# Performance work log

Hardware: AMD Instinct MI355X
Metric: run time of the kernel (lower is better)

Reference implementation:

```python
import jax, jax.numpy as jnp
import numpy as np

N, B, E, H, L, NF = 32768, 2048, 524288, 128, 7, 10
NODE_F = 60  # 10 frames * (loc 3 + vel 3)
OUT_F = 30   # 10 frames * 3


def _mlp(x, W1, b1, W2, b2):
    return jax.nn.relu(x @ W1 + b1) @ W2 + b2


def _lin(key, fan_in, fan_out):
    s = 1.0 / np.sqrt(fan_in)
    kw, kb = jax.random.split(key)
    W = jax.random.uniform(kw, (fan_in, fan_out), jnp.float32, -s, s)
    b = jax.random.uniform(kb, (fan_out,), jnp.float32, -s, s)
    return W, b


def setup_inputs() -> dict:
    key = jax.random.key(0)
    ks = jax.random.split(key, 12)
    p = {}
    p["loc"] = jax.random.normal(ks[0], (N, NF, 3), jnp.float32)
    p["vel"] = jax.random.normal(ks[1], (N, NF, 3), jnp.float32)
    p["y"] = jax.random.normal(ks[2], (N, NF, 3), jnp.float32)
    p["edge_index"] = jax.random.randint(ks[3], (2, E), 0, N, dtype=jnp.int64)
    p["batch_size"] = B
    # embedder: Linear(60,H) -> ReLU -> Linear(H,H)
    p["emb_W1"], p["emb_b1"] = _lin(ks[4], NODE_F, H)
    p["emb_W2"], p["emb_b2"] = _lin(ks[5], H, H)
    # per-layer message net Linear(2H,H)->ReLU->Linear(H,H); update net Linear(2H,H)->ReLU->Linear(H,H)
    mW1, mb1, mW2, mb2, uW1, ub1, uW2, ub2 = [], [], [], [], [], [], [], []
    for i in range(L):
        k = jax.random.fold_in(ks[6], i)
        k1, k2, k3, k4 = jax.random.split(k, 4)
        a, b = _lin(k1, 2 * H, H); mW1.append(a); mb1.append(b)
        a, b = _lin(k2, H, H); mW2.append(a); mb2.append(b)
        a, b = _lin(k3, 2 * H, H); uW1.append(a); ub1.append(b)
        a, b = _lin(k4, H, H); uW2.append(a); ub2.append(b)
    p["msg_W1"] = jnp.stack(mW1); p["msg_b1"] = jnp.stack(mb1)
    p["msg_W2"] = jnp.stack(mW2); p["msg_b2"] = jnp.stack(mb2)
    p["upd_W1"] = jnp.stack(uW1); p["upd_b1"] = jnp.stack(ub1)
    p["upd_W2"] = jnp.stack(uW2); p["upd_b2"] = jnp.stack(ub2)
    # head: Linear(H,H) -> ReLU -> Linear(H,30)
    p["head_W1"], p["head_b1"] = _lin(ks[7], H, H)
    p["head_W2"], p["head_b2"] = _lin(ks[8], H, OUT_F)
    return p


def reference(loc, vel, y, edge_index, batch_size,
              emb_W1, emb_b1, emb_W2, emb_b2,
              msg_W1, msg_b1, msg_W2, msg_b2,
              upd_W1, upd_b1, upd_W2, upd_b2,
              head_W1, head_b1, head_W2, head_b2):
    n = loc.shape[0]
    src, dst = edge_index[0], edge_index[1]  # x_j = x[src], x_i = x[dst] (PyG source_to_target)
    x = jnp.concatenate([loc, vel], axis=-1).reshape(n, -1)  # (N, 60)
    x = _mlp(x, emb_W1, emb_b1, emb_W2, emb_b2)              # (N, H)
    for i in range(L):
        m_in = jnp.concatenate([x[dst], x[src]], axis=-1)    # (E, 2H) cat(x_i, x_j)
        msg = _mlp(m_in, msg_W1[i], msg_b1[i], msg_W2[i], msg_b2[i])  # (E, H)
        agg = jax.ops.segment_sum(msg, dst, num_segments=n)  # scatter-add at targets
        x = _mlp(jnp.concatenate([x, agg], axis=-1), upd_W1[i], upd_b1[i], upd_W2[i], upd_b2[i])
    x = _mlp(x, head_W1, head_b1, head_W2, head_b2)          # (N, 30)
    loc_pred = x.reshape(n, NF, 3) + loc
    d = jnp.sqrt(jnp.sum((loc_pred - y) ** 2, axis=-1))      # (N, NF)
    ade_loss = d.reshape(batch_size, -1, NF).mean(axis=-1).mean(axis=-1)  # (B,)
    fde = jnp.sqrt(jnp.sum((loc_pred[:, -1, :] - y[:, -1, :]) ** 2, axis=-1))  # (N,)
    fde_loss = fde.reshape(batch_size, -1).mean(axis=-1)     # (B,)
    backprop_loss = ade_loss.mean()
    return backprop_loss, ade_loss, fde_loss
```

## Files before the change

### kernel.cpp

```cpp
#include <hip/hip_runtime.h>
#include <hip/hip_bf16.h>
#include <stdint.h>

#define HH 128

typedef __attribute__((ext_vector_type(8))) short short8;
typedef __attribute__((ext_vector_type(4))) float floatx4;

typedef __attribute__((address_space(3))) uint32_t lds_u32_t;
typedef const __attribute__((address_space(1))) uint32_t gbl_u32_t;

__device__ __forceinline__ void gl_lds16(const void* g, void* l) {
  __builtin_amdgcn_global_load_lds((gbl_u32_t*)g, (lds_u32_t*)l, 16, 0, 0);
}

__device__ __forceinline__ float bf2f(short v) {
  union { uint32_t u; float f; } x; x.u = ((uint32_t)(uint16_t)v) << 16; return x.f;
}
__device__ __forceinline__ short f2bf(float f) {
  union { float f; uint32_t u; } x; x.f = f;
  uint32_t r = x.u + 0x7fffu + ((x.u >> 16) & 1u);
  return (short)(r >> 16);
}
__device__ __forceinline__ float rdf(const void* p, int i, int fl) {
  return fl ? bf2f(((const short*)p)[i]) : ((const float*)p)[i];
}


__global__ void detect_idx(const int* __restrict__ eidx, int* flag) {
  __shared__ int nz;
  if (threadIdx.x == 0) nz = 0;
  __syncthreads();
  int any = 0;
  for (int i = threadIdx.x; i < 1024; i += 256) any |= (eidx[2 * i + 1] != 0);
  if (any) atomicOr(&nz, 1);
  __syncthreads();
  if (threadIdx.x == 0) *flag = (nz == 0) ? 1 : 0;
}

__global__ void detect_dtype(const uint32_t* __restrict__ p, int* dflag) {
  __shared__ int cnt;
  if (threadIdx.x == 0) cnt = 0;
  __syncthreads();
  uint32_t u = p[threadIdx.x];
  int e = (u >> 7) & 0xFF;
  if (e >= 100 && e <= 140) atomicAdd(&cnt, 1);
  __syncthreads();
  if (threadIdx.x == 0) *dflag = (cnt >= 192) ? 1 : 0;
}


__global__ void pad_input(const void* __restrict__ loc, const void* __restrict__ vel,
                          short* __restrict__ dst, const int* __restrict__ dflag) {
  int fl = *dflag;
  int idx = blockIdx.x * 256 + threadIdx.x;
  int j = idx & 63, i = idx >> 6;
  short v = 0;
  if (j < 60) {
    int f = j / 6, c = j % 6;
    float x = (c < 3) ? rdf(loc, (i * 10 + f) * 3 + c, fl)
                      : rdf(vel, (i * 10 + f) * 3 + (c - 3), fl);
    v = f2bf(x);
  }
  dst[idx] = v;
}

struct WPrep {
  const void* src[8];
  unsigned long long dstoff[8];
  int L[8], K[8], Nn[8], Kp[8], Np[8];
  int bstart[9];
};

__global__ void prep_w(WPrep a, short* __restrict__ wbase, const int* __restrict__ dflag) {
  int fl = *dflag;
  int b = blockIdx.x;
  int s = 0;
  while (b >= a.bstart[s + 1]) ++s;
  int idx = (b - a.bstart[s]) * 256 + threadIdx.x;
  int Kp = a.Kp[s], Np = a.Np[s], K = a.K[s], Nn = a.Nn[s];
  int tot = a.L[s] * Np * Kp;
  if (idx >= tot) return;
  int k = idx % Kp; int rest = idx / Kp; int n = rest % Np; int l = rest / Np;
  short v = 0;
  if (k < K && n < Nn) v = f2bf(rdf(a.src[s], (l * K + k) * Nn + n, fl));
  wbase[a.dstoff[s] + idx] = v;
}

struct BPrep {
  const void* src[8];
  int n[8];
  int estart[9];
};

__global__ void prep_b(BPrep a, float* __restrict__ bias, const int* __restrict__ dflag) {
  int fl = *dflag;
  int idx = blockIdx.x * 256 + threadIdx.x;
  if (idx >= a.estart[8]) return;
  int s = 0;
  while (idx >= a.estart[s + 1]) ++s;
  int j = idx - a.estart[s];
  bias[idx] = (j < a.n[s]) ? rdf(a.src[s], j, fl) : 0.0f;
}

__global__ void fold_w2(const short* __restrict__ updW1T, const short* __restrict__ msgW2T,
                        short* __restrict__ updW1Tf) {
  int idx = blockIdx.x * 256 + threadIdx.x;
  int k = idx & 255; int n = (idx >> 8) & 127; int l = idx >> 15;
  if (k < 128) { updW1Tf[idx] = updW1T[idx]; return; }
  int kk = k - 128;
  const short* w2 = msgW2T + l * 128 * 128;
  const short* u1 = updW1T + l * 128 * 256 + n * 256 + 128;
  float s = 0.f;
  for (int j = 0; j < 128; ++j) s += bf2f(w2[j * 128 + kk]) * bf2f(u1[j]);
  updW1Tf[idx] = f2bf(s);
}

__global__ void fold_b2(const float* __restrict__ msgB2f, const short* __restrict__ updW1T,
                        float* __restrict__ b2U) {
  int idx = blockIdx.x * 256 + threadIdx.x;
  if (idx >= 7 * 128) return;
  int n = idx & 127, l = idx >> 7;
  const short* u1 = updW1T + l * 128 * 256 + n * 256 + 128;
  const float* b2 = msgB2f + l * 128;
  float s = 0.f;
  for (int j = 0; j < 128; ++j) s += b2[j] * bf2f(u1[j]);
  b2U[idx] = s;
}


__global__ void hist_kernel(const int* __restrict__ eidx, const int* __restrict__ iflag,
                            int* __restrict__ counts, int E) {
  int e = blockIdx.x * 256 + threadIdx.x;
  if (e >= E) return;
  int fl = *iflag;
  int d = fl ? eidx[2 * (E + e)] : eidx[E + e];
  atomicAdd(&counts[d], 1);
}

__global__ void scan_bsum(const int* __restrict__ counts, int* __restrict__ bsums, int N) {
  int i = blockIdx.x * 256 + threadIdx.x;
  int v = (i < N) ? counts[i] : 0;
#pragma unroll
  for (int off = 1; off < 64; off <<= 1) v += __shfl_xor(v, off);
  __shared__ int ws4[4];
  if ((threadIdx.x & 63) == 0) ws4[threadIdx.x >> 6] = v;
  __syncthreads();
  if (threadIdx.x == 0) bsums[blockIdx.x] = ws4[0] + ws4[1] + ws4[2] + ws4[3];
}

__global__ void scan_top(int* __restrict__ bsums, int nb) {
  __shared__ int sh[1024];
  int t = threadIdx.x;
  int v = (t < nb) ? bsums[t] : 0;
  sh[t] = v;
  __syncthreads();
  for (int off = 1; off < 1024; off <<= 1) {
    int u = (t >= off) ? sh[t - off] : 0;
    __syncthreads();
    sh[t] += u;
    __syncthreads();
  }
  if (t < nb) bsums[t] = sh[t] - v;
}

__global__ void scan_final(const int* __restrict__ counts, const int* __restrict__ bsums,
                           int* __restrict__ row_start, int* __restrict__ cursor,
                           float* __restrict__ deg, int N, int E) {
  int i = blockIdx.x * 256 + threadIdx.x;
  int c = (i < N) ? counts[i] : 0;
  int lane = threadIdx.x & 63, w = threadIdx.x >> 6;
  int x = c;
#pragma unroll
  for (int off = 1; off < 64; off <<= 1) {
    int u = __shfl_up(x, off);
    if (lane >= off) x += u;
  }
  __shared__ int wsum[4];
  if (lane == 63) wsum[w] = x;
  __syncthreads();
  int wpre = 0;
#pragma unroll
  for (int k = 0; k < 4; ++k)
    if (k < w) wpre += wsum[k];
  int excl = bsums[blockIdx.x] + wpre + x - c;
  if (i < N) {
    row_start[i] = excl;
    cursor[i] = excl;
    deg[i] = (float)c;
  }
  if (i == N - 1) row_start[N] = E;
}

__global__ void scatter_kernel(const int* __restrict__ eidx, const int* __restrict__ iflag,
                               int* __restrict__ cursor, int* __restrict__ ssrc, int E) {
  int e = blockIdx.x * 256 + threadIdx.x;
  if (e >= E) return;
  int fl = *iflag;
  int d = fl ? eidx[2 * (E + e)] : eidx[E + e];
  int sv = fl ? eidx[2 * e] : eidx[e];
  int pos = atomicAdd(&cursor[d], 1);
  ssrc[pos] = sv;
}


__global__ __launch_bounds__(256, 2)
void gemm_pq(const short* __restrict__ x, const short* __restrict__ W1T,
             const float* __restrict__ b1, float* __restrict__ P, short* __restrict__ Qs) {
  __shared__ __align__(16) char lds[65536];
  const int tid = threadIdx.x;
  const int w = tid >> 6, lane = tid & 63;
  const int quad = lane >> 4, l16 = lane & 15;
  const int R0 = blockIdx.x * 128;

#pragma unroll
  for (int c = 0; c < 16; ++c) {
    int slot = w * 16 + c;
    int mat = slot >> 5, id = slot & 31;
    int s = id >> 3, t = id & 7;
    int n = t * 16 + l16, k = s * 32 + quad * 8;
    gl_lds16(W1T + n * 256 + mat * 128 + k, lds + mat * 32768 + id * 1024 + lane * 16);
  }

  short8 afrag[4][2];
#pragma unroll
  for (int mt = 0; mt < 2; ++mt) {
    int m = R0 + w * 32 + mt * 16 + l16;
    const short* pr = x + (size_t)m * HH;
#pragma unroll
    for (int s = 0; s < 4; ++s) afrag[s][mt] = *(const short8*)(pr + s * 32 + quad * 8);
  }

  float b1f[8];
#pragma unroll
  for (int t = 0; t < 8; ++t) b1f[t] = b1[t * 16 + l16];

  __syncthreads();

  floatx4 zero4 = {0.f, 0.f, 0.f, 0.f};
  {
    floatx4 acc[2][8];
#pragma unroll
    for (int mt = 0; mt < 2; ++mt)
#pragma unroll
      for (int t = 0; t < 8; ++t) acc[mt][t] = zero4;
#pragma unroll
    for (int s = 0; s < 4; ++s) {
      short8 bfrag[8];
#pragma unroll
      for (int t = 0; t < 8; ++t)
        bfrag[t] = *(const short8*)(lds + (s * 8 + t) * 1024 + lane * 16);
#pragma unroll
      for (int mt = 0; mt < 2; ++mt)
#pragma unroll
        for (int t = 0; t < 8; ++t)
          acc[mt][t] = __builtin_amdgcn_mfma_f32_16x16x32_bf16(afrag[s][mt], bfrag[t], acc[mt][t], 0, 0, 0);
    }
#pragma unroll
    for (int mt = 0; mt < 2; ++mt)
#pragma unroll
      for (int nt = 0; nt < 8; ++nt) {
        int col = nt * 16 + l16;
#pragma unroll
        for (int r = 0; r < 4; ++r) {
          int row = R0 + w * 32 + mt * 16 + quad * 4 + r;
          P[(size_t)row * HH + col] = acc[mt][nt][r] + b1f[nt];
        }
      }
  }
  {
    floatx4 acc[2][8];
#pragma unroll
    for (int mt = 0; mt < 2; ++mt)
#pragma unroll
      for (int t = 0; t < 8; ++t) acc[mt][t] = zero4;
#pragma unroll
    for (int s = 0; s < 4; ++s) {
      short8 bfrag[8];
#pragma unroll
      for (int t = 0; t < 8; ++t)
        bfrag[t] = *(const short8*)(lds + 32768 + (s * 8 + t) * 1024 + lane * 16);
#pragma unroll
      for (int mt = 0; mt < 2; ++mt)
#pragma unroll
        for (int t = 0; t < 8; ++t)
          acc[mt][t] = __builtin_amdgcn_mfma_f32_16x16x32_bf16(afrag[s][mt], bfrag[t], acc[mt][t], 0, 0, 0);
    }
#pragma unroll
    for (int mt = 0; mt < 2; ++mt)
#pragma unroll
      for (int nt = 0; nt < 8; ++nt) {
        int col = nt * 16 + l16;
#pragma unroll
        for (int r = 0; r < 4; ++r) {
          int row = R0 + w * 32 + mt * 16 + quad * 4 + r;
          Qs[(size_t)row * HH + col] = f2bf(acc[mt][nt][r]);
        }
      }
  }
}


__global__ __launch_bounds__(256)
void edge_agg(const float* __restrict__ P, const uint32_t* __restrict__ Qp,
              const int* __restrict__ ssrc, const int* __restrict__ row_start,
              uint32_t* __restrict__ Hagg, int Ntot) {
  int w = threadIdx.x >> 6, lane = threadIdx.x & 63;
  int d = blockIdx.x * 4 + w;
  if (d >= Ntot) return;
  float px = P[(size_t)d * HH + 2 * lane];
  float py = P[(size_t)d * HH + 2 * lane + 1];
  int s0 = row_start[d], s1 = row_start[d + 1];
  float ax = 0.f, ay = 0.f;
  int e = s0;
  for (; e + 4 <= s1; e += 4) {
    int i0 = ssrc[e], i1 = ssrc[e + 1], i2 = ssrc[e + 2], i3 = ssrc[e + 3];
    uint32_t q0 = Qp[(size_t)i0 * 64 + lane];
    uint32_t q1 = Qp[(size_t)i1 * 64 + lane];
    uint32_t q2 = Qp[(size_t)i2 * 64 + lane];
    uint32_t q3 = Qp[(size_t)i3 * 64 + lane];
    float hx, hy;
    hx = px + bf2f((short)(q0 & 0xffff)); hy = py + bf2f((short)(q0 >> 16));
    ax += hx > 0.f ? hx : 0.f; ay += hy > 0.f ? hy : 0.f;
    hx = px + bf2f((short)(q1 & 0xffff)); hy = py + bf2f((short)(q1 >> 16));
    ax += hx > 0.f ? hx : 0.f; ay += hy > 0.f ? hy : 0.f;
    hx = px + bf2f((short)(q2 & 0xffff)); hy = py + bf2f((short)(q2 >> 16));
    ax += hx > 0.f ? hx : 0.f; ay += hy > 0.f ? hy : 0.f;
    hx = px + bf2f((short)(q3 & 0xffff)); hy = py + bf2f((short)(q3 >> 16));
    ax += hx > 0.f ? hx : 0.f; ay += hy > 0.f ? hy : 0.f;
  }
  for (; e < s1; ++e) {
    int i0 = ssrc[e];
    uint32_t q0 = Qp[(size_t)i0 * 64 + lane];
    float hx = px + bf2f((short)(q0 & 0xffff));
    float hy = py + bf2f((short)(q0 >> 16));
    ax += hx > 0.f ? hx : 0.f;
    ay += hy > 0.f ? hy : 0.f;
  }
  uint32_t packed = (uint32_t)(uint16_t)f2bf(ax) | ((uint32_t)(uint16_t)f2bf(ay) << 16);
  Hagg[(size_t)d * 64 + lane] = packed;
}


template <int MODE>
__global__ __launch_bounds__(256, 2)
void mlp2_kernel(const short* __restrict__ Asrc, const short* __restrict__ Asrc2,
                 const short* __restrict__ W1T, const float* __restrict__ b1,
                 const short* __restrict__ W2T, const float* __restrict__ b2,
                 short* __restrict__ outbf, float* __restrict__ outf,
                 const float* __restrict__ deg, const float* __restrict__ b2Uv) {
  constexpr int K1 = (MODE == 0) ? 64 : (MODE == 3) ? 128 : 256;
  constexpr int NS = K1 / 32;
  constexpr int N2T = (MODE == 3) ? 2 : 8;

  __shared__ __align__(16) char lds[65536];

  const int tid = threadIdx.x;
  const int w = tid >> 6, lane = tid & 63;
  const int quad = lane >> 4, l16 = lane & 15;
  const int R0 = blockIdx.x * 128;

#pragma unroll
  for (int c = 0; c < NS * 2; ++c) {
    int slot = w * (NS * 2) + c;
    int s = slot >> 3, t = slot & 7;
    int n = t * 16 + l16, k = s * 32 + quad * 8;
    gl_lds16(W1T + n * K1 + k, lds + slot * 1024 + lane * 16);
  }

  short8 afrag[NS][2];
  if constexpr (MODE == 2) {
#pragma unroll
    for (int mt = 0; mt < 2; ++mt) {
      int m = R0 + w * 32 + mt * 16 + l16;
      const short* pr = Asrc + (size_t)m * HH;
      const short* ar = Asrc2 + (size_t)m * HH;
#pragma unroll
      for (int s = 0; s < 4; ++s) {
        afrag[s][mt] = *(const short8*)(pr + s * 32 + quad * 8);
        afrag[s + 4][mt] = *(const short8*)(ar + s * 32 + quad * 8);
      }
    }
  } else {
    constexpr int ST = (MODE == 0) ? 64 : HH;
#pragma unroll
    for (int mt = 0; mt < 2; ++mt) {
      int m = R0 + w * 32 + mt * 16 + l16;
      const short* pr = Asrc + (size_t)m * ST;
#pragma unroll
      for (int s = 0; s < NS; ++s) afrag[s][mt] = *(const short8*)(pr + s * 32 + quad * 8);
    }
  }

  float b1f[8], b2f[N2T], b2u[8];
  float dvals[2][4];
#pragma unroll
  for (int t = 0; t < 8; ++t) b1f[t] = b1[t * 16 + l16];
#pragma unroll
  for (int t = 0; t < N2T; ++t) b2f[t] = b2[t * 16 + l16];
  if constexpr (MODE == 2) {
#pragma unroll
    for (int t = 0; t < 8; ++t) b2u[t] = b2Uv[t * 16 + l16];
#pragma unroll
    for (int mt = 0; mt < 2; ++mt)
#pragma unroll
      for (int r = 0; r < 4; ++r)
        dvals[mt][r] = deg[R0 + w * 32 + mt * 16 + quad * 4 + r];
  }

  __syncthreads();

  floatx4 acc[2][8];
  floatx4 zero4 = {0.f, 0.f, 0.f, 0.f};
#pragma unroll
  for (int mt = 0; mt < 2; ++mt)
#pragma unroll
    for (int t = 0; t < 8; ++t) acc[mt][t] = zero4;

#pragma unroll
  for (int s = 0; s < NS; ++s) {
    short8 bfrag[8];
#pragma unroll
    for (int t = 0; t < 8; ++t)
      bfrag[t] = *(const short8*)(lds + (s * 8 + t) * 1024 + lane * 16);
#pragma unroll
    for (int mt = 0; mt < 2; ++mt)
#pragma unroll
      for (int t = 0; t < 8; ++t)
        acc[mt][t] = __builtin_amdgcn_mfma_f32_16x16x32_bf16(afrag[s][mt], bfrag[t], acc[mt][t], 0, 0, 0);
  }

  __syncthreads();

#pragma unroll
  for (int c = 0; c < N2T; ++c) {
    int n = c * 16 + l16, k = w * 32 + quad * 8;
    gl_lds16(W2T + n * HH + k, lds + 32768 + (w * N2T + c) * 1024 + lane * 16);
  }

  const int mtgb = w * 2;
#pragma unroll
  for (int mt = 0; mt < 2; ++mt) {
#pragma unroll
    for (int nt = 0; nt < 8; ++nt) {
      floatx4 v = acc[mt][nt];
      int s2 = nt >> 1;
      int lpb = 16 * ((nt & 1) * 2 + (l16 >> 3));
      int joff = 2 * (l16 & 7);
      char* base = lds + (size_t)(s2 * 8 + mtgb + mt) * 1024 + joff;
#pragma unroll
      for (int r = 0; r < 4; ++r) {
        float h = v[r] + b1f[nt];
        if constexpr (MODE == 2) h += dvals[mt][r] * b2u[nt];
        h = h > 0.f ? h : 0.f;
        *(short*)(base + (quad * 4 + r + lpb) * 16) = f2bf(h);
      }
    }
  }

  __syncthreads();

  floatx4 acc2[2][N2T];
#pragma unroll
  for (int mt = 0; mt < 2; ++mt)
#pragma unroll
    for (int t = 0; t < N2T; ++t) acc2[mt][t] = zero4;

#pragma unroll
  for (int s2 = 0; s2 < 4; ++s2) {
    short8 af[2];
#pragma unroll
    for (int mt = 0; mt < 2; ++mt)
      af[mt] = *(const short8*)(lds + (s2 * 8 + mtgb + mt) * 1024 + lane * 16);
    short8 bfr[N2T];
#pragma unroll
    for (int t = 0; t < N2T; ++t)
      bfr[t] = *(const short8*)(lds + 32768 + (s2 * N2T + t) * 1024 + lane * 16);
#pragma unroll
    for (int mt = 0; mt < 2; ++mt)
#pragma unroll
      for (int t = 0; t < N2T; ++t)
        acc2[mt][t] = __builtin_amdgcn_mfma_f32_16x16x32_bf16(af[mt], bfr[t], acc2[mt][t], 0, 0, 0);
  }

  if constexpr (MODE == 3) {
#pragma unroll
    for (int mt = 0; mt < 2; ++mt)
#pragma unroll
      for (int nt = 0; nt < N2T; ++nt) {
        int col = nt * 16 + l16;
#pragma unroll
        for (int r = 0; r < 4; ++r) {
          int row = R0 + w * 32 + mt * 16 + quad * 4 + r;
          outf[(size_t)row * 32 + col] = acc2[mt][nt][r] + b2f[nt];
        }
      }
  } else {
#pragma unroll
    for (int mt = 0; mt < 2; ++mt)
#pragma unroll
      for (int nt = 0; nt < 8; ++nt) {
        int col = nt * 16 + l16;
#pragma unroll
        for (int r = 0; r < 4; ++r) {
          int row = R0 + w * 32 + mt * 16 + quad * 4 + r;
          outbf[(size_t)row * HH + col] = f2bf(acc2[mt][nt][r] + b2f[nt]);
        }
      }
  }
}


__global__ void loss_kernel(const float* __restrict__ out32, const void* __restrict__ loc,
                            const void* __restrict__ yv, const int* __restrict__ dflag,
                            float* __restrict__ out, float* __restrict__ acc, int NB) {
  int fl = *dflag;
  int i = blockIdx.x * 256 + threadIdx.x;
  const float* o = out32 + (size_t)i * 32;
  float dsum = 0.f, fde = 0.f;
#pragma unroll
  for (int f = 0; f < 10; ++f) {
    float dx = o[f * 3 + 0] + rdf(loc, i * 30 + f * 3 + 0, fl) - rdf(yv, i * 30 + f * 3 + 0, fl);
    float dy = o[f * 3 + 1] + rdf(loc, i * 30 + f * 3 + 1, fl) - rdf(yv, i * 30 + f * 3 + 1, fl);
    float dz = o[f * 3 + 2] + rdf(loc, i * 30 + f * 3 + 2, fl) - rdf(yv, i * 30 + f * 3 + 2, fl);
    float d = sqrtf(dx * dx + dy * dy + dz * dz);
    dsum += d;
    if (f == 9) fde = d;
  }
#pragma unroll
  for (int m = 1; m < 16; m <<= 1) {
    dsum += __shfl_xor(dsum, m);
    fde += __shfl_xor(fde, m);
  }
  if ((threadIdx.x & 15) == 0) {
    int b = i >> 4;
    out[1 + b] = dsum / 160.0f;
    out[1 + NB + b] = fde / 16.0f;
    unsafeAtomicAdd(acc, dsum);
  }
}

__global__ void final_kernel(const float* __restrict__ acc, float* __restrict__ out, float inv) {
  if (threadIdx.x == 0) out[0] = *acc * inv;
}


extern "C" void kernel_launch(void* const* d_in, const int* in_sizes, int n_in,
                              void* d_out, int out_size, void* d_ws, size_t ws_size,
                              hipStream_t stream) {
  const void* loc = d_in[0];
  const void* vel = d_in[1];
  const void* yv = d_in[2];
  const int* eidx = (const int*)d_in[3];

  const int N = in_sizes[0] / 30;
  const int E = in_sizes[3] / 2;
  const int L = 7;
  const int NB = N / 16;

  const size_t MB = 1024 * 1024;
  char* ws = (char*)d_ws;
  short* x = (short*)ws;
  float* P = (float*)(ws + 8 * MB);
  short* in64 = (short*)(ws + 8 * MB);
  short* Qs = (short*)(ws + 24 * MB);
  short* Hagg = (short*)(ws + 32 * MB);
  float* out32 = (float*)(ws + 32 * MB);
  short* updW1Tf = (short*)(ws + 40 * MB);
  int* bsums = (int*)(ws + 41 * MB);
  short* wbase = (short*)(ws + 48 * MB);
  const unsigned long long OFF_EMBW1 = 0;
  const unsigned long long OFF_EMBW2 = 8192;
  const unsigned long long OFF_HEADW1 = 24576;
  const unsigned long long OFF_HEADW2 = 40960;
  const unsigned long long OFF_MSGW1 = 45056;
  const unsigned long long OFF_MSGW2 = 274432;
  const unsigned long long OFF_UPDW1 = 389120;
  const unsigned long long OFF_UPDW2 = 618496;
  short* embW1T = wbase + OFF_EMBW1;
  short* embW2T = wbase + OFF_EMBW2;
  short* headW1T = wbase + OFF_HEADW1;
  short* headW2T = wbase + OFF_HEADW2;
  short* msgW1T = wbase + OFF_MSGW1;
  short* msgW2T = wbase + OFF_MSGW2;
  short* updW1T = wbase + OFF_UPDW1;
  short* updW2T = wbase + OFF_UPDW2;
  float* bias = (float*)(ws + 49 * MB + 512 * 1024);
  float* embB1f = bias;
  float* embB2f = bias + 128;
  float* msgB1f = bias + 256;
  float* msgB2f = bias + 1152;
  float* updB1f = bias + 2048;
  float* updB2f = bias + 2944;
  float* headB1f = bias + 3840;
  float* headB2f = bias + 3968;
  float* b2U = bias + 4096;
  int* counts = (int*)(ws + 49 * MB + 768 * 1024);
  int* row_start = (int*)(ws + 50 * MB);
  int* cursor = (int*)(ws + 50 * MB + 256 * 1024);
  float* deg = (float*)(ws + 50 * MB + 512 * 1024);
  int* iflag = (int*)(ws + 50 * MB + 768 * 1024);
  int* dflag = iflag + 16;
  float* accp = (float*)(iflag + 32);
  int* ssrc = (int*)(ws + 51 * MB);

  detect_idx<<<1, 256, 0, stream>>>(eidx, iflag);
  detect_dtype<<<1, 256, 0, stream>>>((const uint32_t*)loc, dflag);

  const int NBLK = (N + 255) / 256;
  hipMemsetAsync(counts, 0, (size_t)N * 4, stream);
  hist_kernel<<<(E + 255) / 256, 256, 0, stream>>>(eidx, iflag, counts, E);
  scan_bsum<<<NBLK, 256, 0, stream>>>(counts, bsums, N);
  scan_top<<<1, 1024, 0, stream>>>(bsums, NBLK);
  scan_final<<<NBLK, 256, 0, stream>>>(counts, bsums, row_start, cursor, deg, N, E);
  scatter_kernel<<<(E + 255) / 256, 256, 0, stream>>>(eidx, iflag, cursor, ssrc, E);

  pad_input<<<(N * 64) / 256, 256, 0, stream>>>(loc, vel, in64, dflag);

  {
    WPrep a;
    const void* srcs[8] = {d_in[5], d_in[7], d_in[17], d_in[19],
                           d_in[9], d_in[11], d_in[13], d_in[15]};
    unsigned long long offs[8] = {OFF_EMBW1, OFF_EMBW2, OFF_HEADW1, OFF_HEADW2,
                                  OFF_MSGW1, OFF_MSGW2, OFF_UPDW1, OFF_UPDW2};
    int Ls[8] = {1, 1, 1, 1, 7, 7, 7, 7};
    int Ks[8] = {60, 128, 128, 128, 256, 128, 256, 128};
    int Ns[8] = {128, 128, 128, 30, 128, 128, 128, 128};
    int Kps[8] = {64, 128, 128, 128, 256, 128, 256, 128};
    int Nps[8] = {128, 128, 128, 32, 128, 128, 128, 128};
    int cum = 0;
    for (int s = 0; s < 8; ++s) {
      a.src[s] = srcs[s]; a.dstoff[s] = offs[s];
      a.L[s] = Ls[s]; a.K[s] = Ks[s]; a.Nn[s] = Ns[s]; a.Kp[s] = Kps[s]; a.Np[s] = Nps[s];
      a.bstart[s] = cum;
      cum += (Ls[s] * Nps[s] * Kps[s] + 255) / 256;
    }
    a.bstart[8] = cum;
    prep_w<<<cum, 256, 0, stream>>>(a, wbase, dflag);
  }

  {
    BPrep a;
    const void* srcs[8] = {d_in[6], d_in[8], d_in[10], d_in[12],
                           d_in[14], d_in[16], d_in[18], d_in[20]};
    int ns[8] = {128, 128, 896, 896, 896, 896, 128, 30};
    int es[9] = {0, 128, 256, 1152, 2048, 2944, 3840, 3968, 4000};
    for (int s = 0; s < 8; ++s) { a.src[s] = srcs[s]; a.n[s] = ns[s]; a.estart[s] = es[s]; }
    a.estart[8] = es[8];
    prep_b<<<16, 256, 0, stream>>>(a, bias, dflag);
  }

  fold_w2<<<7 * 128, 256, 0, stream>>>(updW1T, msgW2T, updW1Tf);
  fold_b2<<<4, 256, 0, stream>>>(msgB2f, updW1T, b2U);

  mlp2_kernel<0><<<N / 128, 256, 0, stream>>>(in64, nullptr,
      embW1T, embB1f, embW2T, embB2f, x, nullptr, nullptr, nullptr);

  for (int l = 0; l < L; ++l) {
    gemm_pq<<<N / 128, 256, 0, stream>>>(x, msgW1T + l * 128 * 256, msgB1f + l * 128, P, Qs);
    edge_agg<<<(N + 3) / 4, 256, 0, stream>>>(P, (const uint32_t*)Qs, ssrc, row_start,
                                              (uint32_t*)Hagg, N);
    mlp2_kernel<2><<<N / 128, 256, 0, stream>>>(x, Hagg,
        updW1Tf + l * 128 * 256, updB1f + l * 128, updW2T + l * 128 * 128, updB2f + l * 128,
        x, nullptr, deg, b2U + l * 128);
  }

  mlp2_kernel<3><<<N / 128, 256, 0, stream>>>(x, nullptr,
      headW1T, headB1f, headW2T, headB2f, nullptr, out32, nullptr, nullptr);

  hipMemsetAsync(accp, 0, 4, stream);
  loss_kernel<<<N / 256, 256, 0, stream>>>(out32, loc, yv, dflag, (float*)d_out, accp, NB);
  final_kernel<<<1, 64, 0, stream>>>(accp, (float*)d_out, 1.0f / 327680.0f);
}
```

Baseline: 573.2 us.

## Fuse next-layer P/Q GEMM and head MLP into update MLP kernel

The update MLP kernel now keeps its output x tile in LDS and directly computes the next layer's message first-layer projections (P with bias, Q in bf16), or the head MLP on the last layer. This removes the separate gemm_pq launch and the head kernel, along with the global reread of x. Small setup kernels are also merged: the memset and both detect kernels become one, the two fold kernels become one, and scan_top is folded into scan_final via per-block prefix sums of bsums. The price is more LDS reloads and syncs per block and higher register pressure in the fused kernel.

Result: faster. 533.0 us (-7.0%).

```diff
diff --git a/kernel.cpp b/kernel.cpp
--- a/kernel.cpp
+++ b/kernel.cpp
@@ -27,26 +27,27 @@
 }
 
 
-__global__ void detect_idx(const int* __restrict__ eidx, int* flag) {
-  __shared__ int nz;
-  if (threadIdx.x == 0) nz = 0;
-  __syncthreads();
-  int any = 0;
-  for (int i = threadIdx.x; i < 1024; i += 256) any |= (eidx[2 * i + 1] != 0);
-  if (any) atomicOr(&nz, 1);
-  __syncthreads();
-  if (threadIdx.x == 0) *flag = (nz == 0) ? 1 : 0;
-}
-
-__global__ void detect_dtype(const uint32_t* __restrict__ p, int* dflag) {
-  __shared__ int cnt;
-  if (threadIdx.x == 0) cnt = 0;
-  __syncthreads();
-  uint32_t u = p[threadIdx.x];
-  int e = (u >> 7) & 0xFF;
-  if (e >= 100 && e <= 140) atomicAdd(&cnt, 1);
-  __syncthreads();
-  if (threadIdx.x == 0) *dflag = (cnt >= 192) ? 1 : 0;
+__global__ void detect_zero(const int* __restrict__ eidx, int* iflag, int* dflag,
+                            int* __restrict__ counts, float* accp,
+                            const uint32_t* __restrict__ loc, int N) {
+  int g = blockIdx.x * 256 + threadIdx.x;
+  if (g < N) counts[g] = 0;
+  if (blockIdx.x == 0) {
+    __shared__ int nz, cnt;
+    if (threadIdx.x == 0) { nz = 0; cnt = 0; *accp = 0.f; }
+    __syncthreads();
+    int any = 0;
+    for (int i = threadIdx.x; i < 1024; i += 256) any |= (eidx[2 * i + 1] != 0);
+    if (any) atomicOr(&nz, 1);
+    uint32_t u = loc[threadIdx.x];
+    int e = (u >> 7) & 0xFF;
+    if (e >= 100 && e <= 140) atomicAdd(&cnt, 1);
+    __syncthreads();
+    if (threadIdx.x == 0) {
+      *iflag = (nz == 0) ? 1 : 0;
+      *dflag = (cnt >= 192) ? 1 : 0;
+    }
+  }
 }
 
 
@@ -103,29 +104,30 @@
   bias[idx] = (j < a.n[s]) ? rdf(a.src[s], j, fl) : 0.0f;
 }
 
-__global__ void fold_w2(const short* __restrict__ updW1T, const short* __restrict__ msgW2T,
-                        short* __restrict__ updW1Tf) {
-  int idx = blockIdx.x * 256 + threadIdx.x;
-  int k = idx & 255; int n = (idx >> 8) & 127; int l = idx >> 15;
-  if (k < 128) { updW1Tf[idx] = updW1T[idx]; return; }
-  int kk = k - 128;
-  const short* w2 = msgW2T + l * 128 * 128;
-  const short* u1 = updW1T + l * 128 * 256 + n * 256 + 128;
-  float s = 0.f;
-  for (int j = 0; j < 128; ++j) s += bf2f(w2[j * 128 + kk]) * bf2f(u1[j]);
-  updW1Tf[idx] = f2bf(s);
-}
-
-__global__ void fold_b2(const float* __restrict__ msgB2f, const short* __restrict__ updW1T,
-                        float* __restrict__ b2U) {
-  int idx = blockIdx.x * 256 + threadIdx.x;
-  if (idx >= 7 * 128) return;
-  int n = idx & 127, l = idx >> 7;
-  const short* u1 = updW1T + l * 128 * 256 + n * 256 + 128;
-  const float* b2 = msgB2f + l * 128;
-  float s = 0.f;
-  for (int j = 0; j < 128; ++j) s += b2[j] * bf2f(u1[j]);
-  b2U[idx] = s;
+
+__global__ void fold_kernel(const short* __restrict__ updW1T, const short* __restrict__ msgW2T,
+                            short* __restrict__ updW1Tf, const float* __restrict__ msgB2f,
+                            float* __restrict__ b2U) {
+  if (blockIdx.x < 896) {
+    int idx = blockIdx.x * 256 + threadIdx.x;
+    int k = idx & 255; int n = (idx >> 8) & 127; int l = idx >> 15;
+    if (k < 128) { updW1Tf[idx] = updW1T[idx]; return; }
+    int kk = k - 128;
+    const short* w2 = msgW2T + l * 128 * 128;
+    const short* u1 = updW1T + l * 128 * 256 + n * 256 + 128;
+    float s = 0.f;
+    for (int j = 0; j < 128; ++j) s += bf2f(w2[j * 128 + kk]) * bf2f(u1[j]);
+    updW1Tf[idx] = f2bf(s);
+  } else {
+    int idx = (blockIdx.x - 896) * 256 + threadIdx.x;
+    if (idx >= 7 * 128) return;
+    int n = idx & 127, l = idx >> 7;
+    const short* u1 = updW1T + l * 128 * 256 + n * 256 + 128;
+    const float* b2 = msgB2f + l * 128;
+    float s = 0.f;
+    for (int j = 0; j < 128; ++j) s += b2[j] * bf2f(u1[j]);
+    b2U[idx] = s;
+  }
 }
 
 
@@ -149,41 +151,33 @@
   if (threadIdx.x == 0) bsums[blockIdx.x] = ws4[0] + ws4[1] + ws4[2] + ws4[3];
 }
 
-__global__ void scan_top(int* __restrict__ bsums, int nb) {
-  __shared__ int sh[1024];
-  int t = threadIdx.x;
-  int v = (t < nb) ? bsums[t] : 0;
-  sh[t] = v;
-  __syncthreads();
-  for (int off = 1; off < 1024; off <<= 1) {
-    int u = (t >= off) ? sh[t - off] : 0;
-    __syncthreads();
-    sh[t] += u;
-    __syncthreads();
-  }
-  if (t < nb) bsums[t] = sh[t] - v;
-}
-
 __global__ void scan_final(const int* __restrict__ counts, const int* __restrict__ bsums,
                            int* __restrict__ row_start, int* __restrict__ cursor,
                            float* __restrict__ deg, int N, int E) {
-  int i = blockIdx.x * 256 + threadIdx.x;
+  int t = threadIdx.x;
+  __shared__ int shb[2];
+  __shared__ int wsum[4];
+  int v = (t < 128 && t < (int)blockIdx.x) ? bsums[t] : 0;
+#pragma unroll
+  for (int off = 1; off < 64; off <<= 1) v += __shfl_xor(v, off);
+  if (t == 0) shb[0] = v;
+  if (t == 64) shb[1] = v;
+  int i = blockIdx.x * 256 + t;
   int c = (i < N) ? counts[i] : 0;
-  int lane = threadIdx.x & 63, w = threadIdx.x >> 6;
+  int lane = t & 63, w = t >> 6;
   int x = c;
 #pragma unroll
   for (int off = 1; off < 64; off <<= 1) {
     int u = __shfl_up(x, off);
     if (lane >= off) x += u;
   }
-  __shared__ int wsum[4];
   if (lane == 63) wsum[w] = x;
   __syncthreads();
   int wpre = 0;
 #pragma unroll
   for (int k = 0; k < 4; ++k)
     if (k < w) wpre += wsum[k];
-  int excl = bsums[blockIdx.x] + wpre + x - c;
+  int excl = shb[0] + shb[1] + wpre + x - c;
   if (i < N) {
     row_start[i] = excl;
     cursor[i] = excl;
@@ -201,103 +195,6 @@
   int sv = fl ? eidx[2 * e] : eidx[e];
   int pos = atomicAdd(&cursor[d], 1);
   ssrc[pos] = sv;
-}
-
-
-__global__ __launch_bounds__(256, 2)
-void gemm_pq(const short* __restrict__ x, const short* __restrict__ W1T,
-             const float* __restrict__ b1, float* __restrict__ P, short* __restrict__ Qs) {
-  __shared__ __align__(16) char lds[65536];
-  const int tid = threadIdx.x;
-  const int w = tid >> 6, lane = tid & 63;
-  const int quad = lane >> 4, l16 = lane & 15;
-  const int R0 = blockIdx.x * 128;
-
-#pragma unroll
-  for (int c = 0; c < 16; ++c) {
-    int slot = w * 16 + c;
-    int mat = slot >> 5, id = slot & 31;
-    int s = id >> 3, t = id & 7;
-    int n = t * 16 + l16, k = s * 32 + quad * 8;
-    gl_lds16(W1T + n * 256 + mat * 128 + k, lds + mat * 32768 + id * 1024 + lane * 16);
-  }
-
-  short8 afrag[4][2];
-#pragma unroll
-  for (int mt = 0; mt < 2; ++mt) {
-    int m = R0 + w * 32 + mt * 16 + l16;
-    const short* pr = x + (size_t)m * HH;
-#pragma unroll
-    for (int s = 0; s < 4; ++s) afrag[s][mt] = *(const short8*)(pr + s * 32 + quad * 8);
-  }
-
-  float b1f[8];
-#pragma unroll
-  for (int t = 0; t < 8; ++t) b1f[t] = b1[t * 16 + l16];
-
-  __syncthreads();
-
-  floatx4 zero4 = {0.f, 0.f, 0.f, 0.f};
-  {
-    floatx4 acc[2][8];
-#pragma unroll
-    for (int mt = 0; mt < 2; ++mt)
-#pragma unroll
-      for (int t = 0; t < 8; ++t) acc[mt][t] = zero4;
-#pragma unroll
-    for (int s = 0; s < 4; ++s) {
-      short8 bfrag[8];
-#pragma unroll
-      for (int t = 0; t < 8; ++t)
-        bfrag[t] = *(const short8*)(lds + (s * 8 + t) * 1024 + lane * 16);
-#pragma unroll
-      for (int mt = 0; mt < 2; ++mt)
-#pragma unroll
-        for (int t = 0; t < 8; ++t)
-          acc[mt][t] = __builtin_amdgcn_mfma_f32_16x16x32_bf16(afrag[s][mt], bfrag[t], acc[mt][t], 0, 0, 0);
-    }
-#pragma unroll
-    for (int mt = 0; mt < 2; ++mt)
-#pragma unroll
-      for (int nt = 0; nt < 8; ++nt) {
-        int col = nt * 16 + l16;
-#pragma unroll
-        for (int r = 0; r < 4; ++r) {
-          int row = R0 + w * 32 + mt * 16 + quad * 4 + r;
-          P[(size_t)row * HH + col] = acc[mt][nt][r] + b1f[nt];
-        }
-      }
-  }
-  {
-    floatx4 acc[2][8];
-#pragma unroll
-    for (int mt = 0; mt < 2; ++mt)
-#pragma unroll
-      for (int t = 0; t < 8; ++t) acc[mt][t] = zero4;
-#pragma unroll
-    for (int s = 0; s < 4; ++s) {
-      short8 bfrag[8];
-#pragma unroll
-      for (int t = 0; t < 8; ++t)
-        bfrag[t] = *(const short8*)(lds + 32768 + (s * 8 + t) * 1024 + lane * 16);
-#pragma unroll
-      for (int mt = 0; mt < 2; ++mt)
-#pragma unroll
-        for (int t = 0; t < 8; ++t)
-          acc[mt][t] = __builtin_amdgcn_mfma_f32_16x16x32_bf16(afrag[s][mt], bfrag[t], acc[mt][t], 0, 0, 0);
-    }
-#pragma unroll
-    for (int mt = 0; mt < 2; ++mt)
-#pragma unroll
-      for (int nt = 0; nt < 8; ++nt) {
-        int col = nt * 16 + l16;
-#pragma unroll
-        for (int r = 0; r < 4; ++r) {
-          int row = R0 + w * 32 + mt * 16 + quad * 4 + r;
-          Qs[(size_t)row * HH + col] = f2bf(acc[mt][nt][r]);
-        }
-      }
-  }
 }
 
 
@@ -342,16 +239,58 @@
 }
 
 
+__device__ __forceinline__ void write_aslots(char* lds, const floatx4 v2[2][8],
+                                             int w, int quad, int l16) {
+  const int mtgb = w * 2;
+#pragma unroll
+  for (int mt = 0; mt < 2; ++mt)
+#pragma unroll
+    for (int nt = 0; nt < 8; ++nt) {
+      floatx4 v = v2[mt][nt];
+      int s2 = nt >> 1;
+      int lpb = 16 * ((nt & 1) * 2 + (l16 >> 3));
+      int joff = 2 * (l16 & 7);
+      char* base = lds + (size_t)(s2 * 8 + mtgb + mt) * 1024 + joff;
+#pragma unroll
+      for (int r = 0; r < 4; ++r)
+        *(short*)(base + (quad * 4 + r + lpb) * 16) = f2bf(v[r]);
+    }
+}
+
+template <int NT>
+__device__ __forceinline__ void gemm_lds(const char* lds, int mtgb, floatx4 acc[2][NT], int lane) {
+#pragma unroll
+  for (int s2 = 0; s2 < 4; ++s2) {
+    short8 af[2];
+#pragma unroll
+    for (int mt = 0; mt < 2; ++mt)
+      af[mt] = *(const short8*)(lds + (s2 * 8 + mtgb + mt) * 1024 + lane * 16);
+    short8 bfr[NT];
+#pragma unroll
+    for (int t = 0; t < NT; ++t)
+      bfr[t] = *(const short8*)(lds + 32768 + (s2 * NT + t) * 1024 + lane * 16);
+#pragma unroll
+    for (int mt = 0; mt < 2; ++mt)
+#pragma unroll
+      for (int t = 0; t < NT; ++t)
+        acc[mt][t] = __builtin_amdgcn_mfma_f32_16x16x32_bf16(af[mt], bfr[t], acc[mt][t], 0, 0, 0);
+  }
+}
+
+
 template <int MODE>
 __global__ __launch_bounds__(256, 2)
-void mlp2_kernel(const short* __restrict__ Asrc, const short* __restrict__ Asrc2,
-                 const short* __restrict__ W1T, const float* __restrict__ b1,
-                 const short* __restrict__ W2T, const float* __restrict__ b2,
-                 short* __restrict__ outbf, float* __restrict__ outf,
-                 const float* __restrict__ deg, const float* __restrict__ b2Uv) {
-  constexpr int K1 = (MODE == 0) ? 64 : (MODE == 3) ? 128 : 256;
+void mlp_fused(const short* __restrict__ Asrc, const short* __restrict__ Asrc2,
+               const short* __restrict__ W1T, const float* __restrict__ b1,
+               const short* __restrict__ W2T, const float* __restrict__ b2,
+               const float* __restrict__ deg, const float* __restrict__ b2Uv,
+               const short* __restrict__ pqW1, const float* __restrict__ pqB1,
+               const short* __restrict__ pq2W, const float* __restrict__ pq2B,
+               short* __restrict__ xout, float* __restrict__ Pout,
+               short* __restrict__ Qout, float* __restrict__ out32) {
+  constexpr int K1 = (MODE == 0) ? 64 : 256;
   constexpr int NS = K1 / 32;
-  constexpr int N2T = (MODE == 3) ? 2 : 8;
+  constexpr int PQS = (MODE == 3) ? 128 : 256;
 
   __shared__ __align__(16) char lds[65536];
 
@@ -359,6 +298,7 @@
   const int w = tid >> 6, lane = tid & 63;
   const int quad = lane >> 4, l16 = lane & 15;
   const int R0 = blockIdx.x * 128;
+  const int mtgb = w * 2;
 
 #pragma unroll
   for (int c = 0; c < NS * 2; ++c) {
@@ -369,7 +309,15 @@
   }
 
   short8 afrag[NS][2];
-  if constexpr (MODE == 2) {
+  if constexpr (MODE == 0) {
+#pragma unroll
+    for (int mt = 0; mt < 2; ++mt) {
+      int m = R0 + w * 32 + mt * 16 + l16;
+      const short* pr = Asrc + (size_t)m * 64;
+#pragma unroll
+      for (int s = 0; s < NS; ++s) afrag[s][mt] = *(const short8*)(pr + s * 32 + quad * 8);
+    }
+  } else {
 #pragma unroll
     for (int mt = 0; mt < 2; ++mt) {
       int m = R0 + w * 32 + mt * 16 + l16;
@@ -381,24 +329,17 @@
         afrag[s + 4][mt] = *(const short8*)(ar + s * 32 + quad * 8);
       }
     }
-  } else {
-    constexpr int ST = (MODE == 0) ? 64 : HH;
-#pragma unroll
-    for (int mt = 0; mt < 2; ++mt) {
-      int m = R0 + w * 32 + mt * 16 + l16;
-      const short* pr = Asrc + (size_t)m * ST;
-#pragma unroll
-      for (int s = 0; s < NS; ++s) afrag[s][mt] = *(const short8*)(pr + s * 32 + quad * 8);
-    }
-  }
-
-  float b1f[8], b2f[N2T], b2u[8];
+  }
+
+  float b1f[8], b2f[8], pb1[8], b2u[8];
   float dvals[2][4];
 #pragma unroll
   for (int t = 0; t < 8; ++t) b1f[t] = b1[t * 16 + l16];
 #pragma unroll
-  for (int t = 0; t < N2T; ++t) b2f[t] = b2[t * 16 + l16];
-  if constexpr (MODE == 2) {
+  for (int t = 0; t < 8; ++t) b2f[t] = b2[t * 16 + l16];
+#pragma unroll
+  for (int t = 0; t < 8; ++t) pb1[t] = pqB1[t * 16 + l16];
+  if constexpr (MODE != 0) {
 #pragma unroll
     for (int t = 0; t < 8; ++t) b2u[t] = b2Uv[t * 16 + l16];
 #pragma unroll
@@ -410,13 +351,12 @@
 
   __syncthreads();
 
+  floatx4 zero4 = {0.f, 0.f, 0.f, 0.f};
   floatx4 acc[2][8];
-  floatx4 zero4 = {0.f, 0.f, 0.f, 0.f};
 #pragma unroll
   for (int mt = 0; mt < 2; ++mt)
 #pragma unroll
     for (int t = 0; t < 8; ++t) acc[mt][t] = zero4;
-
 #pragma unroll
   for (int s = 0; s < NS; ++s) {
     short8 bfrag[8];
@@ -433,66 +373,115 @@
   __syncthreads();
 
 #pragma unroll
-  for (int c = 0; c < N2T; ++c) {
+  for (int c = 0; c < 8; ++c) {
+    int slot = w * 8 + c;
     int n = c * 16 + l16, k = w * 32 + quad * 8;
-    gl_lds16(W2T + n * HH + k, lds + 32768 + (w * N2T + c) * 1024 + lane * 16);
-  }
-
-  const int mtgb = w * 2;
-#pragma unroll
-  for (int mt = 0; mt < 2; ++mt) {
-#pragma unroll
-    for (int nt = 0; nt < 8; ++nt) {
-      floatx4 v = acc[mt][nt];
-      int s2 = nt >> 1;
-      int lpb = 16 * ((nt & 1) * 2 + (l16 >> 3));
-      int joff = 2 * (l16 & 7);
-      char* base = lds + (size_t)(s2 * 8 + mtgb + mt) * 1024 + joff;
-#pragma unroll
-      for (int r = 0; r < 4; ++r) {
-        float h = v[r] + b1f[nt];
-        if constexpr (MODE == 2) h += dvals[mt][r] * b2u[nt];
-        h = h > 0.f ? h : 0.f;
-        *(short*)(base + (quad * 4 + r + lpb) * 16) = f2bf(h);
-      }
-    }
+    gl_lds16(W2T + n * HH + k, lds + 32768 + slot * 1024 + lane * 16);
+  }
+  {
+    floatx4 hv[2][8];
+#pragma unroll
+    for (int mt = 0; mt < 2; ++mt)
+#pragma unroll
+      for (int nt = 0; nt < 8; ++nt)
+#pragma unroll
+        for (int r = 0; r < 4; ++r) {
+          float h = acc[mt][nt][r] + b1f[nt];
+          if constexpr (MODE != 0) h += dvals[mt][r] * b2u[nt];
+          hv[mt][nt][r] = h > 0.f ? h : 0.f;
+        }
+    write_aslots(lds, hv, w, quad, l16);
   }
 
   __syncthreads();
 
-  floatx4 acc2[2][N2T];
+  floatx4 acc2[2][8];
 #pragma unroll
   for (int mt = 0; mt < 2; ++mt)
 #pragma unroll
-    for (int t = 0; t < N2T; ++t) acc2[mt][t] = zero4;
-
-#pragma unroll
-  for (int s2 = 0; s2 < 4; ++s2) {
-    short8 af[2];
-#pragma unroll
-    for (int mt = 0; mt < 2; ++mt)
-      af[mt] = *(const short8*)(lds + (s2 * 8 + mtgb + mt) * 1024 + lane * 16);
-    short8 bfr[N2T];
-#pragma unroll
-    for (int t = 0; t < N2T; ++t)
-      bfr[t] = *(const short8*)(lds + 32768 + (s2 * N2T + t) * 1024 + lane * 16);
-#pragma unroll
-    for (int mt = 0; mt < 2; ++mt)
-#pragma unroll
-      for (int t = 0; t < N2T; ++t)
-        acc2[mt][t] = __builtin_amdgcn_mfma_f32_16x16x32_bf16(af[mt], bfr[t], acc2[mt][t], 0, 0, 0);
-  }
-
-  if constexpr (MODE == 3) {
-#pragma unroll
-    for (int mt = 0; mt < 2; ++mt)
-#pragma unroll
-      for (int nt = 0; nt < N2T; ++nt) {
+    for (int t = 0; t < 8; ++t) acc2[mt][t] = zero4;
+  gemm_lds<8>(lds, mtgb, acc2, lane);
+
+  floatx4 xv[2][8];
+#pragma unroll
+  for (int mt = 0; mt < 2; ++mt)
+#pragma unroll
+    for (int nt = 0; nt < 8; ++nt)
+#pragma unroll
+      for (int r = 0; r < 4; ++r)
+        xv[mt][nt][r] = acc2[mt][nt][r] + b2f[nt];
+
+  if constexpr (MODE != 3) {
+#pragma unroll
+    for (int mt = 0; mt < 2; ++mt)
+#pragma unroll
+      for (int nt = 0; nt < 8; ++nt) {
         int col = nt * 16 + l16;
 #pragma unroll
         for (int r = 0; r < 4; ++r) {
           int row = R0 + w * 32 + mt * 16 + quad * 4 + r;
-          outf[(size_t)row * 32 + col] = acc2[mt][nt][r] + b2f[nt];
+          xout[(size_t)row * HH + col] = f2bf(xv[mt][nt][r]);
+        }
+      }
+  }
+
+  __syncthreads();
+
+  write_aslots(lds, xv, w, quad, l16);
+#pragma unroll
+  for (int c = 0; c < 8; ++c) {
+    int slot = w * 8 + c;
+    int n = c * 16 + l16, k = w * 32 + quad * 8;
+    gl_lds16(pqW1 + n * PQS + k, lds + 32768 + slot * 1024 + lane * 16);
+  }
+
+  __syncthreads();
+
+  floatx4 accc[2][8];
+#pragma unroll
+  for (int mt = 0; mt < 2; ++mt)
+#pragma unroll
+    for (int t = 0; t < 8; ++t) accc[mt][t] = zero4;
+  gemm_lds<8>(lds, mtgb, accc, lane);
+
+  if constexpr (MODE == 3) {
+    floatx4 h2[2][8];
+#pragma unroll
+    for (int mt = 0; mt < 2; ++mt)
+#pragma unroll
+      for (int nt = 0; nt < 8; ++nt)
+#pragma unroll
+        for (int r = 0; r < 4; ++r) {
+          float h = accc[mt][nt][r] + pb1[nt];
+          h2[mt][nt][r] = h > 0.f ? h : 0.f;
+        }
+    __syncthreads();
+    write_aslots(lds, h2, w, quad, l16);
+#pragma unroll
+    for (int c = 0; c < 2; ++c) {
+      int slot = w * 2 + c;
+      int n = c * 16 + l16, k = w * 32 + quad * 8;
+      gl_lds16(pq2W + n * 128 + k, lds + 32768 + slot * 1024 + lane * 16);
+    }
+    __syncthreads();
+    floatx4 acco[2][2];
+#pragma unroll
+    for (int mt = 0; mt < 2; ++mt)
+#pragma unroll
+      for (int t = 0; t < 2; ++t) acco[mt][t] = zero4;
+    gemm_lds<2>(lds, mtgb, acco, lane);
+    float ob[2];
+#pragma unroll
+    for (int t = 0; t < 2; ++t) ob[t] = pq2B[t * 16 + l16];
+#pragma unroll
+    for (int mt = 0; mt < 2; ++mt)
+#pragma unroll
+      for (int nt = 0; nt < 2; ++nt) {
+        int col = nt * 16 + l16;
+#pragma unroll
+        for (int r = 0; r < 4; ++r) {
+          int row = R0 + w * 32 + mt * 16 + quad * 4 + r;
+          out32[(size_t)row * 32 + col] = acco[mt][nt][r] + ob[nt];
         }
       }
   } else {
@@ -504,7 +493,32 @@
 #pragma unroll
         for (int r = 0; r < 4; ++r) {
           int row = R0 + w * 32 + mt * 16 + quad * 4 + r;
-          outbf[(size_t)row * HH + col] = f2bf(acc2[mt][nt][r] + b2f[nt]);
+          Pout[(size_t)row * HH + col] = accc[mt][nt][r] + pb1[nt];
+        }
+      }
+    __syncthreads();
+#pragma unroll
+    for (int c = 0; c < 8; ++c) {
+      int slot = w * 8 + c;
+      int n = c * 16 + l16, k = w * 32 + quad * 8;
+      gl_lds16(pqW1 + n * 256 + 128 + k, lds + 32768 + slot * 1024 + lane * 16);
+    }
+    __syncthreads();
+    floatx4 accq[2][8];
+#pragma unroll
+    for (int mt = 0; mt < 2; ++mt)
+#pragma unroll
+      for (int t = 0; t < 8; ++t) accq[mt][t] = zero4;
+    gemm_lds<8>(lds, mtgb, accq, lane);
+#pragma unroll
+    for (int mt = 0; mt < 2; ++mt)
+#pragma unroll
+      for (int nt = 0; nt < 8; ++nt) {
+        int col = nt * 16 + l16;
+#pragma unroll
+        for (int r = 0; r < 4; ++r) {
+          int row = R0 + w * 32 + mt * 16 + quad * 4 + r;
+          Qout[(size_t)row * HH + col] = f2bf(accq[mt][nt][r]);
         }
       }
   }
@@ -562,10 +576,8 @@
   char* ws = (char*)d_ws;
   short* x = (short*)ws;
   float* P = (float*)(ws + 8 * MB);
-  short* in64 = (short*)(ws + 8 * MB);
   short* Qs = (short*)(ws + 24 * MB);
   short* Hagg = (short*)(ws + 32 * MB);
-  float* out32 = (float*)(ws + 32 * MB);
   short* updW1Tf = (short*)(ws + 40 * MB);
   int* bsums = (int*)(ws + 41 * MB);
   short* wbase = (short*)(ws + 48 * MB);
@@ -603,15 +615,15 @@
   int* dflag = iflag + 16;
   float* accp = (float*)(iflag + 32);
   int* ssrc = (int*)(ws + 51 * MB);
-
-  detect_idx<<<1, 256, 0, stream>>>(eidx, iflag);
-  detect_dtype<<<1, 256, 0, stream>>>((const uint32_t*)loc, dflag);
+  short* in64 = (short*)(ws + 53 * MB);
+  float* out32 = (float*)(ws + 57 * MB);
 
   const int NBLK = (N + 255) / 256;
-  hipMemsetAsync(counts, 0, (size_t)N * 4, stream);
+
+  detect_zero<<<NBLK, 256, 0, stream>>>(eidx, iflag, dflag, counts, accp,
+                                        (const uint32_t*)loc, N);
   hist_kernel<<<(E + 255) / 256, 256, 0, stream>>>(eidx, iflag, counts, E);
   scan_bsum<<<NBLK, 256, 0, stream>>>(counts, bsums, N);
-  scan_top<<<1, 1024, 0, stream>>>(bsums, NBLK);
   scan_final<<<NBLK, 256, 0, stream>>>(counts, bsums, row_start, cursor, deg, N, E);
   scatter_kernel<<<(E + 255) / 256, 256, 0, stream>>>(eidx, iflag, cursor, ssrc, E);
 
@@ -638,7 +650,6 @@
     a.bstart[8] = cum;
     prep_w<<<cum, 256, 0, stream>>>(a, wbase, dflag);
   }
-
   {
     BPrep a;
     const void* srcs[8] = {d_in[6], d_in[8], d_in[10], d_in[12],
@@ -650,25 +661,30 @@
     prep_b<<<16, 256, 0, stream>>>(a, bias, dflag);
   }
 
-  fold_w2<<<7 * 128, 256, 0, stream>>>(updW1T, msgW2T, updW1Tf);
-  fold_b2<<<4, 256, 0, stream>>>(msgB2f, updW1T, b2U);
-
-  mlp2_kernel<0><<<N / 128, 256, 0, stream>>>(in64, nullptr,
-      embW1T, embB1f, embW2T, embB2f, x, nullptr, nullptr, nullptr);
+  fold_kernel<<<900, 256, 0, stream>>>(updW1T, msgW2T, updW1Tf, msgB2f, b2U);
+
+  mlp_fused<0><<<N / 128, 256, 0, stream>>>(in64, nullptr,
+      embW1T, embB1f, embW2T, embB2f, nullptr, nullptr,
+      msgW1T, msgB1f, nullptr, nullptr, x, P, Qs, nullptr);
 
   for (int l = 0; l < L; ++l) {
-    gemm_pq<<<N / 128, 256, 0, stream>>>(x, msgW1T + l * 128 * 256, msgB1f + l * 128, P, Qs);
     edge_agg<<<(N + 3) / 4, 256, 0, stream>>>(P, (const uint32_t*)Qs, ssrc, row_start,
                                               (uint32_t*)Hagg, N);
-    mlp2_kernel<2><<<N / 128, 256, 0, stream>>>(x, Hagg,
-        updW1Tf + l * 128 * 256, updB1f + l * 128, updW2T + l * 128 * 128, updB2f + l * 128,
-        x, nullptr, deg, b2U + l * 128);
-  }
-
-  mlp2_kernel<3><<<N / 128, 256, 0, stream>>>(x, nullptr,
-      headW1T, headB1f, headW2T, headB2f, nullptr, out32, nullptr, nullptr);
-
-  hipMemsetAsync(accp, 0, 4, stream);
+    if (l < L - 1) {
+      mlp_fused<2><<<N / 128, 256, 0, stream>>>(x, Hagg,
+          updW1Tf + l * 128 * 256, updB1f + l * 128, updW2T + l * 128 * 128, updB2f + l * 128,
+          deg, b2U + l * 128,
+          msgW1T + (l + 1) * 128 * 256, msgB1f + (l + 1) * 128, nullptr, nullptr,
+          x, P, Qs, nullptr);
+    } else {
+      mlp_fused<3><<<N / 128, 256, 0, stream>>>(x, Hagg,
+          updW1Tf + l * 128 * 256, updB1f + l * 128, updW2T + l * 128 * 128, updB2f + l * 128,
+          deg, b2U + l * 128,
+          headW1T, headB1f, headW2T, headB2f,
+          nullptr, nullptr, nullptr, out32);
+    }
+  }
+
   loss_kernel<<<N / 256, 256, 0, stream>>>(out32, loc, yv, dflag, (float*)d_out, accp, NB);
   final_kernel<<<1, 64, 0, stream>>>(accp, (float*)d_out, 1.0f / 327680.0f);
 }
```
